# Kernel tuning notes

Measured on AMD Instinct MI355X. Metric: run time of the kernel, lower is better.

## Reference

```python
import jax, jax.numpy as jnp
import numpy as np

N = 100000
E = 1600000
IN_FEATS = 512
DIMS = [128, 128, 64]
NEG_SLOPE_ATT = 0.2   # PyG GATConv default
NEG_SLOPE_ACT = 0.25  # F.leaky_relu in GAT.forward


def setup_inputs() -> dict:
    key = jax.random.key(0)
    ks = jax.random.split(key, 16)
    inp = {
        "data": jax.random.normal(ks[0], (N, IN_FEATS), dtype=jnp.float32),
        "adj": jax.random.randint(ks[1], (2, E), 0, N, dtype=jnp.int64),
    }
    dims_in = [IN_FEATS] + DIMS[:-1]
    ki = 2
    for l, (di, do) in enumerate(zip(dims_in, DIMS), start=1):
        scale = 1.0 / np.sqrt(di)
        inp[f"W{l}"] = jax.random.normal(ks[ki], (di, do), dtype=jnp.float32) * scale; ki += 1
        inp[f"a_src{l}"] = jax.random.normal(ks[ki], (do,), dtype=jnp.float32) * 0.1; ki += 1
        inp[f"a_dst{l}"] = jax.random.normal(ks[ki], (do,), dtype=jnp.float32) * 0.1; ki += 1
        inp[f"b{l}"] = jnp.zeros((do,), dtype=jnp.float32)
    return inp


def gat_conv(x, src, dst, W, a_src, a_dst, b):
    h = x @ W                                        # [N, do]
    alpha_s = h @ a_src                              # [N]
    alpha_d = h @ a_dst                              # [N]
    logits = jax.nn.leaky_relu(alpha_s[src] + alpha_d[dst], NEG_SLOPE_ATT)  # [E']
    # segment softmax over edges sharing the same destination node
    m = jax.ops.segment_max(logits, dst, num_segments=N)
    e = jnp.exp(logits - m[dst])
    s = jax.ops.segment_sum(e, dst, num_segments=N)
    alpha = e / s[dst]                               # [E']
    out = jax.ops.segment_sum(alpha[:, None] * h[src], dst, num_segments=N)
    return out + b


def reference(data, adj, W1, a_src1, a_dst1, b1, W2, a_src2, a_dst2, b2, W3, a_src3, a_dst3, b3):
    # PyG GATConv adds self-loops by default
    loops = jnp.arange(N, dtype=adj.dtype)
    src = jnp.concatenate([adj[0], loops])
    dst = jnp.concatenate([adj[1], loops])
    x = data
    x = jax.nn.leaky_relu(gat_conv(x, src, dst, W1, a_src1, a_dst1, b1), NEG_SLOPE_ACT)
    x = jax.nn.leaky_relu(gat_conv(x, src, dst, W2, a_src2, a_dst2, b2), NEG_SLOPE_ACT)
    x = jax.nn.leaky_relu(gat_conv(x, src, dst, W3, a_src3, a_dst3, b3), NEG_SLOPE_ACT)
    return x
```

## Files before the change

kernel.cpp:

```cpp
#include <hip/hip_runtime.h>

typedef unsigned short u16;
typedef unsigned int u32;
typedef short short8 __attribute__((ext_vector_type(8)));
typedef float floatx4 __attribute__((ext_vector_type(4)));

__device__ __forceinline__ u16 f2bf(float x) {
    u32 u = __float_as_uint(x);
    u += 0x7fffu + ((u >> 16) & 1u);
    return (u16)(u >> 16);
}

__global__ void zero_out_k(float* __restrict__ out, int n) {
    int i = blockIdx.x * 256 + threadIdx.x;
    if (i < n) out[i] = 0.f;
}


__global__ void hist_k(const int* __restrict__ dst, int* __restrict__ cnt, int E, int N) {
    int e = blockIdx.x * 256 + threadIdx.x;
    if (e < E) {
        int d = dst[e];
        d = d < 0 ? 0 : (d >= N ? N - 1 : d);
        atomicAdd(&cnt[d], 1);
    }
}

__global__ void scan1_k(const int* __restrict__ cnt, int* __restrict__ excl,
                        int* __restrict__ aux, int N) {
    __shared__ int tmp[1024];
    int t = threadIdx.x;
    int i = blockIdx.x * 1024 + t;
    int v = (i < N) ? cnt[i] : 0;
    tmp[t] = v;
    __syncthreads();
    for (int off = 1; off < 1024; off <<= 1) {
        int x = (t >= off) ? tmp[t - off] : 0;
        __syncthreads();
        tmp[t] += x;
        __syncthreads();
    }
    if (i < N) excl[i] = tmp[t] - v;
    if (t == 1023) aux[blockIdx.x] = tmp[t];
}

__global__ void scan2_k(int* __restrict__ aux, int nb) {
    int lane = threadIdx.x;
    int v0 = (lane < nb) ? aux[lane] : 0;
    int v1 = (lane + 64 < nb) ? aux[lane + 64] : 0;
    int s0 = v0;
    for (int off = 1; off < 64; off <<= 1) { int x = __shfl_up(s0, off); if (lane >= off) s0 += x; }
    int total0 = __shfl(s0, 63);
    int s1 = v1;
    for (int off = 1; off < 64; off <<= 1) { int x = __shfl_up(s1, off); if (lane >= off) s1 += x; }
    if (lane < nb) aux[lane] = s0 - v0;
    if (lane + 64 < nb) aux[lane + 64] = total0 + s1 - v1;
}

__global__ void scan3_k(const int* __restrict__ excl, const int* __restrict__ aux,
                        int* __restrict__ offs, int* __restrict__ cursor, int N, int E) {
    int i = blockIdx.x * 1024 + threadIdx.x;
    if (i < N) {
        int v = excl[i] + aux[blockIdx.x];
        offs[i] = v;
        cursor[i] = v;
    } else if (i == N) {
        offs[N] = E;
    }
}

__global__ void scatter_k(const int* __restrict__ src, const int* __restrict__ dst,
                          int* __restrict__ cursor, int* __restrict__ esrc, int E, int N) {
    int e = blockIdx.x * 256 + threadIdx.x;
    if (e < E) {
        int d = dst[e];
        d = d < 0 ? 0 : (d >= N ? N - 1 : d);
        int s = src[e];
        s = s < 0 ? 0 : (s >= N ? N - 1 : s);
        int p = atomicAdd(&cursor[d], 1);
        esrc[p] = s;
    }
}

__global__ void prepack_k(const float* __restrict__ W, u16* __restrict__ Wf, int DO, int total) {
    int idx = blockIdx.x * 256 + threadIdx.x;
    if (idx >= total) return;
    int j = idx & 7;
    int t = idx >> 3;
    int n = t % DO;
    int kq = t / DO;
    Wf[idx] = f2bf(W[(size_t)(kq * 8 + j) * DO + n]);
}

template <int K, int DO, bool F32IN>
__global__ __launch_bounds__(256, 2) void gemm_k(const void* __restrict__ Xv,
                                                 const u16* __restrict__ Wf,
                                                 float* __restrict__ H, int nrow) {
    constexpr int BM = 128, BK = 64;
    __shared__ alignas(16) u16 At[BM * BK];
    const int tid = threadIdx.x;
    const int wave = tid >> 6, lane = tid & 63;
    const int quad = lane >> 4, l16 = lane & 15;
    const int row0 = blockIdx.x * BM;

    floatx4 acc[2][DO / 16];
#pragma unroll
    for (int a = 0; a < 2; a++)
#pragma unroll
        for (int b = 0; b < DO / 16; b++) acc[a][b] = floatx4{0.f, 0.f, 0.f, 0.f};

    for (int kt = 0; kt < K / BK; ++kt) {
        __syncthreads();
#pragma unroll
        for (int i = 0; i < 4; ++i) {
            int seg = tid + i * 256;
            int r = seg >> 3, c = seg & 7;
            int gr = row0 + r;
            gr = gr < nrow ? gr : nrow - 1;
            u16 pk[8];
            if (F32IN) {
                const float* X = (const float*)Xv;
                float4 v0 = *(const float4*)(X + (size_t)gr * K + kt * BK + c * 8);
                float4 v1 = *(const float4*)(X + (size_t)gr * K + kt * BK + c * 8 + 4);
                pk[0] = f2bf(v0.x); pk[1] = f2bf(v0.y); pk[2] = f2bf(v0.z); pk[3] = f2bf(v0.w);
                pk[4] = f2bf(v1.x); pk[5] = f2bf(v1.y); pk[6] = f2bf(v1.z); pk[7] = f2bf(v1.w);
                *(int4*)(At + r * BK + (c ^ (r & 7)) * 8) = *(const int4*)pk;
            } else {
                const u16* X = (const u16*)Xv;
                int4 v = *(const int4*)(X + (size_t)gr * K + kt * BK + c * 8);
                *(int4*)(At + r * BK + (c ^ (r & 7)) * 8) = v;
            }
        }
        __syncthreads();
#pragma unroll
        for (int ks = 0; ks < 2; ++ks) {
            short8 bfr[DO / 16];
            int kq = kt * 8 + ks * 4 + quad;
#pragma unroll
            for (int ct = 0; ct < DO / 16; ++ct)
                bfr[ct] = *(const short8*)(Wf + ((size_t)kq * DO + ct * 16 + l16) * 8);
#pragma unroll
            for (int rt = 0; rt < 2; ++rt) {
                int row = wave * 32 + rt * 16 + l16;
                int unit = (ks * 4 + quad) ^ (row & 7);
                short8 afr = *(const short8*)(At + row * BK + unit * 8);
#pragma unroll
                for (int ct = 0; ct < DO / 16; ++ct)
                    acc[rt][ct] =
                        __builtin_amdgcn_mfma_f32_16x16x32_bf16(afr, bfr[ct], acc[rt][ct], 0, 0, 0);
            }
        }
    }
#pragma unroll
    for (int rt = 0; rt < 2; ++rt)
#pragma unroll
        for (int r = 0; r < 4; ++r) {
            int grow = row0 + wave * 32 + rt * 16 + quad * 4 + r;
            if (grow < nrow) {
#pragma unroll
                for (int ct = 0; ct < DO / 16; ++ct)
                    H[(size_t)grow * DO + ct * 16 + l16] = acc[rt][ct][r];
            }
        }
}

template <int DO>
__global__ __launch_bounds__(256) void alphas_k(const float* __restrict__ H,
                                                const float* __restrict__ a_src,
                                                const float* __restrict__ a_dst,
                                                float* __restrict__ AS, float* __restrict__ AD,
                                                int N) {
    int wave = threadIdx.x >> 6, lane = threadIdx.x & 63;
    int n = blockIdx.x * 4 + wave;
    if (n >= N) return;
    float ps = 0.f, pd = 0.f;
#pragma unroll
    for (int f = lane; f < DO; f += 64) {
        float h = H[(size_t)n * DO + f];
        ps += h * a_src[f];
        pd += h * a_dst[f];
    }
    for (int o = 32; o; o >>= 1) {
        ps += __shfl_xor(ps, o);
        pd += __shfl_xor(pd, o);
    }
    if (lane == 0) {
        AS[n] = ps;
        AD[n] = pd;
    }
}

template <int DO, bool OUTB>
__global__ __launch_bounds__(256) void agg_k(const float* __restrict__ H,
                                             const float* __restrict__ AS,
                                             const float* __restrict__ AD,
                                             const int* __restrict__ offs,
                                             const int* __restrict__ esrc,
                                             const float* __restrict__ bias,
                                             void* __restrict__ OUT, int N) {
    const int wave = threadIdx.x >> 6, lane = threadIdx.x & 63;
    const int d = blockIdx.x * 4 + wave;
    if (d >= N) return;
    const int o0 = offs[d];
    const int deg = offs[d + 1] - o0;
    const int tot = deg + 1;
    const float ad = AD[d];

    float mx = -1e30f;
    for (int i = lane; i < tot; i += 64) {
        int s = (i < deg) ? esrc[o0 + i] : d;
        float lg = AS[s] + ad;
        lg = lg > 0.f ? lg : lg * 0.2f;
        mx = fmaxf(mx, lg);
    }
    for (int o = 32; o; o >>= 1) mx = fmaxf(mx, __shfl_xor(mx, o));

    float sum = 0.f;
    for (int i = lane; i < tot; i += 64) {
        int s = (i < deg) ? esrc[o0 + i] : d;
        float lg = AS[s] + ad;
        lg = lg > 0.f ? lg : lg * 0.2f;
        sum += __expf(lg - mx);
    }
    for (int o = 32; o; o >>= 1) sum += __shfl_xor(sum, o);
    const float inv = 1.f / sum;

    float acc0 = 0.f, acc1 = 0.f;
    for (int c0 = 0; c0 < tot; c0 += 64) {
        int i = c0 + lane;
        float w = 0.f;
        int s = d;
        if (i < tot) {
            s = (i < deg) ? esrc[o0 + i] : d;
            float lg = AS[s] + ad;
            lg = lg > 0.f ? lg : lg * 0.2f;
            w = __expf(lg - mx) * inv;
        }
        int cn = tot - c0;
        cn = cn < 64 ? cn : 64;
        for (int l = 0; l < cn; ++l) {
            float wl = __shfl(w, l);
            int sl = __shfl(s, l);
            if (DO == 128) {
                float2 hv = *(const float2*)(H + (size_t)sl * 128 + 2 * lane);
                acc0 = fmaf(wl, hv.x, acc0);
                acc1 = fmaf(wl, hv.y, acc1);
            } else {
                acc0 = fmaf(wl, H[(size_t)sl * DO + lane], acc0);
            }
        }
    }

    if (DO == 128) {
        int f = 2 * lane;
        float v0 = acc0 + bias[f];
        float v1 = acc1 + bias[f + 1];
        v0 = v0 > 0.f ? v0 : v0 * 0.25f;
        v1 = v1 > 0.f ? v1 : v1 * 0.25f;
        if (OUTB) {
            u32 packed = (u32)f2bf(v0) | ((u32)f2bf(v1) << 16);
            ((u32*)OUT)[(size_t)d * 64 + lane] = packed;
        } else {
            ((float2*)OUT)[(size_t)d * 64 + lane] = float2{v0, v1};
        }
    } else {
        float v0 = acc0 + bias[lane];
        v0 = v0 > 0.f ? v0 : v0 * 0.25f;
        if (OUTB) {
            ((u16*)OUT)[(size_t)d * DO + lane] = f2bf(v0);
        } else {
            ((float*)OUT)[(size_t)d * DO + lane] = v0;
        }
    }
}


extern "C" void kernel_launch(void* const* d_in, const int* in_sizes, int n_in,
                              void* d_out, int out_size, void* d_ws, size_t ws_size,
                              hipStream_t stream) {
    const int N = in_sizes[0] / 512;
    const int E = in_sizes[1] / 2;

    const float* data = (const float*)d_in[0];
    const int* adj = (const int*)d_in[1];
    const float* W1 = (const float*)d_in[2];
    const float* as1 = (const float*)d_in[3];
    const float* ad1 = (const float*)d_in[4];
    const float* b1 = (const float*)d_in[5];
    const float* W2 = (const float*)d_in[6];
    const float* as2 = (const float*)d_in[7];
    const float* ad2 = (const float*)d_in[8];
    const float* b2 = (const float*)d_in[9];
    const float* W3 = (const float*)d_in[10];
    const float* as3 = (const float*)d_in[11];
    const float* ad3 = (const float*)d_in[12];
    const float* b3 = (const float*)d_in[13];

    char* ws = (char*)d_ws;
    size_t need = 0;
    auto carve = [&](size_t bytes) {
        void* p = (void*)(ws + need);
        need += (bytes + 255) & ~(size_t)255;
        return p;
    };
    int* esrc = (int*)carve((size_t)E * 4);
    int* offs = (int*)carve((size_t)(N + 1) * 4);
    int* cursor = (int*)carve((size_t)N * 4);
    int* cnt = (int*)carve((size_t)N * 4);
    int* excl = (int*)carve((size_t)N * 4);
    int* aux = (int*)carve(1024);
    float* AS = (float*)carve((size_t)N * 4);
    float* AD = (float*)carve((size_t)N * 4);
    float* h = (float*)carve((size_t)N * 128 * 4);
    u16* x1 = (u16*)carve((size_t)N * 128 * 2);
    u16* x2 = x1;
    u16* Wf1 = (u16*)carve(512 * 128 * 2);
    u16* Wf2 = (u16*)carve(128 * 128 * 2);
    u16* Wf3 = (u16*)carve(128 * 64 * 2);

    if (need > ws_size) {
        zero_out_k<<<(out_size + 255) / 256, 256, 0, stream>>>((float*)d_out, out_size);
        return;
    }

    const int* srcl = adj;
    const int* dstl = adj + E;

    hipMemsetAsync(cnt, 0, (size_t)N * 4, stream);
    hist_k<<<(E + 255) / 256, 256, 0, stream>>>(dstl, cnt, E, N);
    int nb = (N + 1023) / 1024;
    scan1_k<<<nb, 1024, 0, stream>>>(cnt, excl, aux, N);
    scan2_k<<<1, 64, 0, stream>>>(aux, nb);
    scan3_k<<<nb, 1024, 0, stream>>>(excl, aux, offs, cursor, N, E);
    scatter_k<<<(E + 255) / 256, 256, 0, stream>>>(srcl, dstl, cursor, esrc, E, N);

    prepack_k<<<(512 * 128 + 255) / 256, 256, 0, stream>>>(W1, Wf1, 128, 512 * 128);
    prepack_k<<<(128 * 128 + 255) / 256, 256, 0, stream>>>(W2, Wf2, 128, 128 * 128);
    prepack_k<<<(128 * 64 + 255) / 256, 256, 0, stream>>>(W3, Wf3, 64, 128 * 64);

    const int gblk = (N + 127) / 128;
    const int nblk = (N + 3) / 4;

    gemm_k<512, 128, true><<<gblk, 256, 0, stream>>>(data, Wf1, h, N);
    alphas_k<128><<<nblk, 256, 0, stream>>>(h, as1, ad1, AS, AD, N);
    agg_k<128, true><<<nblk, 256, 0, stream>>>(h, AS, AD, offs, esrc, b1, x1, N);
    gemm_k<128, 128, false><<<gblk, 256, 0, stream>>>(x1, Wf2, h, N);
    alphas_k<128><<<nblk, 256, 0, stream>>>(h, as2, ad2, AS, AD, N);
    agg_k<128, true><<<nblk, 256, 0, stream>>>(h, AS, AD, offs, esrc, b2, x2, N);
    gemm_k<128, 64, false><<<gblk, 256, 0, stream>>>(x2, Wf3, h, N);
    alphas_k<64><<<nblk, 256, 0, stream>>>(h, as3, ad3, AS, AD, N);
    agg_k<64, false><<<nblk, 256, 0, stream>>>(h, AS, AD, offs, esrc, b3, d_out, N);
}
```

Before: 1.025 ms.

## Fuse attention logits into GEMM epilogue, store H in bf16, single-pass softmax

Computes the per-node source and destination attention scores inside the GEMM epilogue with a 16-lane shuffle reduction, which removes the separate alphas kernels and their reread of H. H for layers 1 and 2 is stored as bf16, halving the bytes gathered per edge in aggregation. Layer 3 keeps fp32 H. Aggregation gains a fast path for in-degree up to 63 that computes max, sum and weights in one pass instead of three passes over the edge list. The bf16 H adds rounding error to the attention weights and features.

```diff
diff --git a/kernel.cpp b/kernel.cpp
--- a/kernel.cpp
+++ b/kernel.cpp
@@ -5,6 +5,7 @@
 typedef short short8 __attribute__((ext_vector_type(8)));
 typedef float floatx4 __attribute__((ext_vector_type(4)));
 
+__device__ __forceinline__ float bf2f(u16 x) { return __uint_as_float(((u32)x) << 16); }
 __device__ __forceinline__ u16 f2bf(float x) {
     u32 u = __float_as_uint(x);
     u += 0x7fffu + ((u >> 16) & 1u);
@@ -92,10 +93,14 @@
     Wf[idx] = f2bf(W[(size_t)(kq * 8 + j) * DO + n]);
 }
 
-template <int K, int DO, bool F32IN>
+template <int K, int DO, bool F32IN, bool H32>
 __global__ __launch_bounds__(256, 2) void gemm_k(const void* __restrict__ Xv,
                                                  const u16* __restrict__ Wf,
-                                                 float* __restrict__ H, int nrow) {
+                                                 void* __restrict__ Hv,
+                                                 const float* __restrict__ a_src,
+                                                 const float* __restrict__ a_dst,
+                                                 float* __restrict__ AS,
+                                                 float* __restrict__ AD, int nrow) {
     constexpr int BM = 128, BK = 64;
     __shared__ alignas(16) u16 At[BM * BK];
     const int tid = threadIdx.x;
@@ -151,47 +156,45 @@
             }
         }
     }
+    float asv[DO / 16], adv[DO / 16];
+#pragma unroll
+    for (int ct = 0; ct < DO / 16; ++ct) {
+        asv[ct] = a_src[ct * 16 + l16];
+        adv[ct] = a_dst[ct * 16 + l16];
+    }
 #pragma unroll
     for (int rt = 0; rt < 2; ++rt)
 #pragma unroll
         for (int r = 0; r < 4; ++r) {
             int grow = row0 + wave * 32 + rt * 16 + quad * 4 + r;
-            if (grow < nrow) {
-#pragma unroll
-                for (int ct = 0; ct < DO / 16; ++ct)
-                    H[(size_t)grow * DO + ct * 16 + l16] = acc[rt][ct][r];
-            }
-        }
-}
-
-template <int DO>
-__global__ __launch_bounds__(256) void alphas_k(const float* __restrict__ H,
-                                                const float* __restrict__ a_src,
-                                                const float* __restrict__ a_dst,
-                                                float* __restrict__ AS, float* __restrict__ AD,
-                                                int N) {
-    int wave = threadIdx.x >> 6, lane = threadIdx.x & 63;
-    int n = blockIdx.x * 4 + wave;
-    if (n >= N) return;
-    float ps = 0.f, pd = 0.f;
-#pragma unroll
-    for (int f = lane; f < DO; f += 64) {
-        float h = H[(size_t)n * DO + f];
-        ps += h * a_src[f];
-        pd += h * a_dst[f];
-    }
-    for (int o = 32; o; o >>= 1) {
-        ps += __shfl_xor(ps, o);
-        pd += __shfl_xor(pd, o);
-    }
-    if (lane == 0) {
-        AS[n] = ps;
-        AD[n] = pd;
-    }
-}
-
-template <int DO, bool OUTB>
-__global__ __launch_bounds__(256) void agg_k(const float* __restrict__ H,
+            bool ok = grow < nrow;
+            float ps = 0.f, pd = 0.f;
+#pragma unroll
+            for (int ct = 0; ct < DO / 16; ++ct) {
+                float v = acc[rt][ct][r];
+                ps = fmaf(v, asv[ct], ps);
+                pd = fmaf(v, adv[ct], pd);
+                if (ok) {
+                    if (H32)
+                        ((float*)Hv)[(size_t)grow * DO + ct * 16 + l16] = v;
+                    else
+                        ((u16*)Hv)[(size_t)grow * DO + ct * 16 + l16] = f2bf(v);
+                }
+            }
+#pragma unroll
+            for (int o = 1; o < 16; o <<= 1) {
+                ps += __shfl_xor(ps, o);
+                pd += __shfl_xor(pd, o);
+            }
+            if (ok && l16 == 0) {
+                AS[grow] = ps;
+                AD[grow] = pd;
+            }
+        }
+}
+
+template <int DO, bool HB, bool OUTB>
+__global__ __launch_bounds__(256) void agg_k(const void* __restrict__ Hv,
                                              const float* __restrict__ AS,
                                              const float* __restrict__ AD,
                                              const int* __restrict__ offs,
@@ -206,47 +209,91 @@
     const int tot = deg + 1;
     const float ad = AD[d];
 
-    float mx = -1e30f;
-    for (int i = lane; i < tot; i += 64) {
-        int s = (i < deg) ? esrc[o0 + i] : d;
+    float acc0 = 0.f, acc1 = 0.f;
+
+    if (tot <= 64) {
+        int s = (lane < deg) ? esrc[o0 + lane] : d;
+        bool valid = lane < tot;
         float lg = AS[s] + ad;
         lg = lg > 0.f ? lg : lg * 0.2f;
-        mx = fmaxf(mx, lg);
-    }
-    for (int o = 32; o; o >>= 1) mx = fmaxf(mx, __shfl_xor(mx, o));
-
-    float sum = 0.f;
-    for (int i = lane; i < tot; i += 64) {
-        int s = (i < deg) ? esrc[o0 + i] : d;
-        float lg = AS[s] + ad;
-        lg = lg > 0.f ? lg : lg * 0.2f;
-        sum += __expf(lg - mx);
-    }
-    for (int o = 32; o; o >>= 1) sum += __shfl_xor(sum, o);
-    const float inv = 1.f / sum;
-
-    float acc0 = 0.f, acc1 = 0.f;
-    for (int c0 = 0; c0 < tot; c0 += 64) {
-        int i = c0 + lane;
-        float w = 0.f;
-        int s = d;
-        if (i < tot) {
-            s = (i < deg) ? esrc[o0 + i] : d;
-            float lg = AS[s] + ad;
-            lg = lg > 0.f ? lg : lg * 0.2f;
-            w = __expf(lg - mx) * inv;
-        }
-        int cn = tot - c0;
-        cn = cn < 64 ? cn : 64;
-        for (int l = 0; l < cn; ++l) {
+        float lgv = valid ? lg : -1e30f;
+        float m = lgv;
+        for (int o = 32; o; o >>= 1) m = fmaxf(m, __shfl_xor(m, o));
+        float e = valid ? __expf(lg - m) : 0.f;
+        float sum = e;
+        for (int o = 32; o; o >>= 1) sum += __shfl_xor(sum, o);
+        float w = e * (1.f / sum);
+        for (int l = 0; l < tot; ++l) {
             float wl = __shfl(w, l);
             int sl = __shfl(s, l);
             if (DO == 128) {
-                float2 hv = *(const float2*)(H + (size_t)sl * 128 + 2 * lane);
-                acc0 = fmaf(wl, hv.x, acc0);
-                acc1 = fmaf(wl, hv.y, acc1);
+                if (HB) {
+                    u32 hv = ((const u32*)Hv)[(size_t)sl * 64 + lane];
+                    acc0 = fmaf(wl, bf2f((u16)hv), acc0);
+                    acc1 = fmaf(wl, bf2f((u16)(hv >> 16)), acc1);
+                } else {
+                    float2 hv = ((const float2*)Hv)[(size_t)sl * 64 + lane];
+                    acc0 = fmaf(wl, hv.x, acc0);
+                    acc1 = fmaf(wl, hv.y, acc1);
+                }
             } else {
-                acc0 = fmaf(wl, H[(size_t)sl * DO + lane], acc0);
+                if (HB) {
+                    acc0 = fmaf(wl, bf2f(((const u16*)Hv)[(size_t)sl * DO + lane]), acc0);
+                } else {
+                    acc0 = fmaf(wl, ((const float*)Hv)[(size_t)sl * DO + lane], acc0);
+                }
+            }
+        }
+    } else {
+        float mx = -1e30f;
+        for (int i = lane; i < tot; i += 64) {
+            int s = (i < deg) ? esrc[o0 + i] : d;
+            float lg = AS[s] + ad;
+            lg = lg > 0.f ? lg : lg * 0.2f;
+            mx = fmaxf(mx, lg);
+        }
+        for (int o = 32; o; o >>= 1) mx = fmaxf(mx, __shfl_xor(mx, o));
+        float sum = 0.f;
+        for (int i = lane; i < tot; i += 64) {
+            int s = (i < deg) ? esrc[o0 + i] : d;
+            float lg = AS[s] + ad;
+            lg = lg > 0.f ? lg : lg * 0.2f;
+            sum += __expf(lg - mx);
+        }
+        for (int o = 32; o; o >>= 1) sum += __shfl_xor(sum, o);
+        const float inv = 1.f / sum;
+        for (int c0 = 0; c0 < tot; c0 += 64) {
+            int i = c0 + lane;
+            float w = 0.f;
+            int s = d;
+            if (i < tot) {
+                s = (i < deg) ? esrc[o0 + i] : d;
+                float lg = AS[s] + ad;
+                lg = lg > 0.f ? lg : lg * 0.2f;
+                w = __expf(lg - mx) * inv;
+            }
+            int cn = tot - c0;
+            cn = cn < 64 ? cn : 64;
+            for (int l = 0; l < cn; ++l) {
+                float wl = __shfl(w, l);
+                int sl = __shfl(s, l);
+                if (DO == 128) {
+                    if (HB) {
+                        u32 hv = ((const u32*)Hv)[(size_t)sl * 64 + lane];
+                        acc0 = fmaf(wl, bf2f((u16)hv), acc0);
+                        acc1 = fmaf(wl, bf2f((u16)(hv >> 16)), acc1);
+                    } else {
+                        float2 hv = ((const float2*)Hv)[(size_t)sl * 64 + lane];
+                        acc0 = fmaf(wl, hv.x, acc0);
+                        acc1 = fmaf(wl, hv.y, acc1);
+                    }
+                } else {
+                    if (HB) {
+                        acc0 = fmaf(wl, bf2f(((const u16*)Hv)[(size_t)sl * DO + lane]), acc0);
+                    } else {
+                        acc0 = fmaf(wl, ((const float*)Hv)[(size_t)sl * DO + lane], acc0);
+                    }
+                }
             }
         }
     }
@@ -311,7 +358,8 @@
     int* aux = (int*)carve(1024);
     float* AS = (float*)carve((size_t)N * 4);
     float* AD = (float*)carve((size_t)N * 4);
-    float* h = (float*)carve((size_t)N * 128 * 4);
+    u16* Hb = (u16*)carve((size_t)N * 128 * 2);
+    float* H32 = (float*)Hb;
     u16* x1 = (u16*)carve((size_t)N * 128 * 2);
     u16* x2 = x1;
     u16* Wf1 = (u16*)carve(512 * 128 * 2);
@@ -341,13 +389,10 @@
     const int gblk = (N + 127) / 128;
     const int nblk = (N + 3) / 4;
 
-    gemm_k<512, 128, true><<<gblk, 256, 0, stream>>>(data, Wf1, h, N);
-    alphas_k<128><<<nblk, 256, 0, stream>>>(h, as1, ad1, AS, AD, N);
-    agg_k<128, true><<<nblk, 256, 0, stream>>>(h, AS, AD, offs, esrc, b1, x1, N);
-    gemm_k<128, 128, false><<<gblk, 256, 0, stream>>>(x1, Wf2, h, N);
-    alphas_k<128><<<nblk, 256, 0, stream>>>(h, as2, ad2, AS, AD, N);
-    agg_k<128, true><<<nblk, 256, 0, stream>>>(h, AS, AD, offs, esrc, b2, x2, N);
-    gemm_k<128, 64, false><<<gblk, 256, 0, stream>>>(x2, Wf3, h, N);
-    alphas_k<64><<<nblk, 256, 0, stream>>>(h, as3, ad3, AS, AD, N);
-    agg_k<64, false><<<nblk, 256, 0, stream>>>(h, AS, AD, offs, esrc, b3, d_out, N);
-}
+    gemm_k<512, 128, true, false><<<gblk, 256, 0, stream>>>(data, Wf1, Hb, as1, ad1, AS, AD, N);
+    agg_k<128, true, true><<<nblk, 256, 0, stream>>>(Hb, AS, AD, offs, esrc, b1, x1, N);
+    gemm_k<128, 128, false, false><<<gblk, 256, 0, stream>>>(x1, Wf2, Hb, as2, ad2, AS, AD, N);
+    agg_k<128, true, true><<<nblk, 256, 0, stream>>>(Hb, AS, AD, offs, esrc, b2, x2, N);
+    gemm_k<128, 64, false, true><<<gblk, 256, 0, stream>>>(x2, Wf3, H32, as3, ad3, AS, AD, N);
+    agg_k<64, false, false><<<nblk, 256, 0, stream>>>(H32, AS, AD, offs, esrc, b3, d_out, N);
+}
```

Measured after the change: 925.7 us. 9.7% less time.
